# Kernel optimization log

Measured on AMD Instinct MI355X. Metric: run time of the kernel, lower is better.

## Reference

```python
import jax, jax.numpy as jnp
import numpy as np

N = 50000      # num nodes (spots)
E = 800000     # num edges before self-loops
IN = 3000      # input_dim (HVGs)
HID = 512      # hidden_dim
LAT = 30       # latent_dim
HEADS = 1
NEG_SLOPE = 0.2


def setup_inputs() -> dict:
    key = jax.random.key(0)
    ks = jax.random.split(key, 8)
    x = jax.random.normal(ks[0], (N, IN), jnp.float32)
    edge_index = jax.random.randint(ks[1], (2, E), 0, N)
    edge_attr = jax.random.uniform(ks[2], (E,), jnp.float32)
    # parameters (Xavier-ish scales)
    enc_w1 = jax.random.normal(ks[3], (HID, IN), jnp.float32) * (1.0 / np.sqrt(IN))
    enc_b1 = jnp.zeros((HID,), jnp.float32)
    gat_w = jax.random.normal(ks[4], (HID, HEADS * LAT), jnp.float32) * (1.0 / np.sqrt(HID))
    gat_att = jax.random.normal(ks[5], (HEADS, 2 * LAT), jnp.float32) * 0.1
    gat_b = jnp.zeros((LAT,), jnp.float32)
    dec_w1 = jax.random.normal(ks[6], (HID, LAT), jnp.float32) * (1.0 / np.sqrt(LAT))
    dec_b1 = jnp.zeros((HID,), jnp.float32)
    dec_b2 = jnp.zeros((IN,), jnp.float32)
    return dict(x=x, edge_index=edge_index, edge_attr=edge_attr,
                enc_w1=enc_w1, enc_b1=enc_b1, gat_w=gat_w, gat_att=gat_att,
                gat_b=gat_b, dec_w1=dec_w1, dec_b1=dec_b1, dec_b2=dec_b2)


def _gat_layer(h, src, dst, eattr, gat_w, gat_att, gat_b):
    """GAT layer: Eq.5-7, concat=False (mean over heads), multiplicative edge_attr."""
    xh = (h @ gat_w).reshape(N, HEADS, LAT)          # W h, per head
    x_i = xh[dst]                                     # target node feats (E+N, H, LAT)
    x_j = xh[src]                                     # source node feats
    att_i, att_j = gat_att[:, :LAT], gat_att[:, LAT:]
    # e_ij = LeakyReLU(a^T [Wh_i || Wh_j])
    alpha = jnp.einsum('ehc,hc->eh', x_i, att_i) + jnp.einsum('ehc,hc->eh', x_j, att_j)
    alpha = jax.nn.leaky_relu(alpha, NEG_SLOPE)
    alpha = alpha * eattr[:, None]                    # edge weight applied pre-softmax
    # segment softmax over incoming edges of each target node (self-loops ensure non-empty)
    amax = jax.ops.segment_max(alpha, dst, num_segments=N)
    alpha = jnp.exp(alpha - amax[dst])
    denom = jax.ops.segment_sum(alpha, dst, num_segments=N)
    alpha = alpha / (denom[dst] + 1e-16)
    # h'_i = sum_j alpha_ij * W h_j
    msg = x_j * alpha[:, :, None]                     # (E+N, H, LAT)
    out = jax.ops.segment_sum(msg, dst, num_segments=N)  # (N, H, LAT)
    return out.mean(axis=1) + gat_b                   # concat=False -> mean over heads


def reference(x, edge_index, edge_attr, enc_w1, enc_b1, gat_w, gat_att, gat_b,
              dec_w1, dec_b1, dec_b2):
    # add self-loops with fill_value=1.0
    loops = jnp.arange(N, dtype=edge_index.dtype)
    src = jnp.concatenate([edge_index[0], loops])
    dst = jnp.concatenate([edge_index[1], loops])
    eattr = jnp.concatenate([edge_attr, jnp.ones((N,), edge_attr.dtype)])

    # encoder: fc1 -> ELU -> GAT -> ELU
    h = jax.nn.elu(x @ enc_w1.T + enc_b1)
    z = jax.nn.elu(_gat_layer(h, src, dst, eattr, gat_w, gat_att, gat_b))

    # decoder: fc1 -> ELU -> tied fc2 (W^b = W^T, own bias)
    hd = jax.nn.elu(z @ dec_w1.T + dec_b1)
    x_recon = hd @ enc_w1 + dec_b2
    return (x_recon, z)
```

## Files before the change

### kernel.cpp

```cpp
#include <hip/hip_runtime.h>
#include <hip/hip_bf16.h>
#include <math.h>

#define N_NODES 50000
#define E_EDGES 800000
#define ET (E_EDGES + N_NODES)
#define IN_DIM 3000
#define HID 512
#define LAT 30
#define XH_STRIDE 32
#define NEG_SLOPE 0.2f
#define KPAD 3072
#define ENC_NT 94
#define DEC_NT 16
#define APITCH 40

typedef __bf16 bfv8 __attribute__((ext_vector_type(8)));
typedef float f32x4 __attribute__((ext_vector_type(4)));

__device__ __forceinline__ float eluf(float x) { return x > 0.f ? x : expm1f(x); }

__device__ __forceinline__ unsigned fkey(float f) {
    unsigned u = __float_as_uint(f);
    return (u & 0x80000000u) ? ~u : (u | 0x80000000u);
}
__device__ __forceinline__ float funkey(unsigned k) {
    unsigned u = (k & 0x80000000u) ? (k ^ 0x80000000u) : ~k;
    return __uint_as_float(u);
}

__global__ void k_init(float* __restrict__ zbuf, unsigned* __restrict__ amax, float* __restrict__ denom) {
    int gid = blockIdx.x * 256 + threadIdx.x;
    if (gid < N_NODES * XH_STRIDE) zbuf[gid] = 0.f;
    if (gid < N_NODES) { amax[gid] = 0u; denom[gid] = 0.f; }
}

__global__ void k_transpose_w(const float* __restrict__ w, float* __restrict__ wt) {
    int idx = blockIdx.x * 256 + threadIdx.x;
    if (idx < HID * LAT) {
        int j = idx / LAT, c = idx % LAT;
        wt[c * HID + j] = w[idx];
    }
}

__global__ void k_conv_w(const float* __restrict__ w, __bf16* __restrict__ w1b, __bf16* __restrict__ w1bt) {
    int idx = blockIdx.x * 256 + threadIdx.x;
    if (idx >= HID * KPAD) return;
    int j = idx / KPAD, k = idx - j * KPAD;
    float v = (k < IN_DIM) ? w[(size_t)j * IN_DIM + k] : 0.f;
    __bf16 b = (__bf16)v;
    w1b[(size_t)j * KPAD + k] = b;
    w1bt[(size_t)k * HID + j] = b;
}

__global__ __launch_bounds__(256)
void k_enc_gemm(const float* __restrict__ A, const __bf16* __restrict__ Bb,
                const float* __restrict__ bias, float* __restrict__ C) {
    __shared__ __bf16 As[2][128 * APITCH];
    __shared__ __bf16 Bs[3][4096];
    const int tid = threadIdx.x;
    const int lane = tid & 63, wv = tid >> 6;
    const int wr = wv >> 1, wc = wv & 1;
    const int l16 = lane & 15, lh = lane >> 4;
    const int p = ((int)blockIdx.y >> 2) * 8 + (int)blockIdx.x;
    if (p > 390) return;
    const int i0 = p * 128;
    const int c0 = ((int)blockIdx.y & 3) * 128;

    const int arow = tid >> 2, akc = tid & 3;
    const int r0 = i0 + arow, r1 = i0 + arow + 64;
    const float* apA = A + (size_t)(r0 < N_NODES ? r0 : N_NODES - 1) * IN_DIM + akc * 8;
    const float* apB = A + (size_t)(r1 < N_NODES ? r1 : N_NODES - 1) * IN_DIM + akc * 8;

    f32x4 acc[4][4] = {};
    float4 a00, a01, a10, a11;

    auto stageB = [&](int kt, int b) {
#pragma unroll
        for (int s = 0; s < 2; ++s) {
            int g = wv * 2 + s;
            int ks = g >> 1;
            int col = (g & 1) * 64 + (lane ^ (ks << 1));
            const __bf16* src = Bb + (size_t)(c0 + col) * KPAD + kt + ks * 8;
            __builtin_amdgcn_global_load_lds(
                (const __attribute__((address_space(1))) void*)src,
                (__attribute__((address_space(3))) void*)(&Bs[b][(size_t)g * 512]),
                16, 0, 0);
        }
    };
    auto loadA = [&](int kt) {
        a00 = a01 = a10 = a11 = make_float4(0.f, 0.f, 0.f, 0.f);
        if (kt + akc * 8 < IN_DIM) {
            const float4* p0 = (const float4*)(apA + kt);
            a00 = p0[0]; a01 = p0[1];
            const float4* p1 = (const float4*)(apB + kt);
            a10 = p1[0]; a11 = p1[1];
        }
    };
    auto writeA = [&](int b) {
        bfv8 pk;
        pk[0] = (__bf16)a00.x; pk[1] = (__bf16)a00.y; pk[2] = (__bf16)a00.z; pk[3] = (__bf16)a00.w;
        pk[4] = (__bf16)a01.x; pk[5] = (__bf16)a01.y; pk[6] = (__bf16)a01.z; pk[7] = (__bf16)a01.w;
        *(bfv8*)&As[b][(size_t)arow * APITCH + akc * 8] = pk;
        pk[0] = (__bf16)a10.x; pk[1] = (__bf16)a10.y; pk[2] = (__bf16)a10.z; pk[3] = (__bf16)a10.w;
        pk[4] = (__bf16)a11.x; pk[5] = (__bf16)a11.y; pk[6] = (__bf16)a11.z; pk[7] = (__bf16)a11.w;
        *(bfv8*)&As[b][(size_t)(arow + 64) * APITCH + akc * 8] = pk;
    };

    stageB(0, 0);
    stageB(32, 1);
    loadA(0);
    writeA(0);
    asm volatile("s_waitcnt vmcnt(0) lgkmcnt(0)" ::: "memory");
    __builtin_amdgcn_s_barrier();
    __builtin_amdgcn_sched_barrier(0);

    int acur = 0;
    for (int t = 0; t < ENC_NT; ++t) {
        const int bt = t % 3;
        const bool nxt1 = (t + 1) < ENC_NT, nxt2 = (t + 2) < ENC_NT;
        if (nxt1) loadA((t + 1) * 32);
        if (nxt2) stageB((t + 2) * 32, (t + 2) % 3);

        bfv8 af[4], bfr[4];
#pragma unroll
        for (int mi = 0; mi < 4; ++mi)
            af[mi] = *(const bfv8*)&As[acur][(size_t)(wr * 64 + mi * 16 + l16) * APITCH + lh * 8];
#pragma unroll
        for (int ni = 0; ni < 4; ++ni)
            bfr[ni] = *(const bfv8*)&Bs[bt][((size_t)lh * 128 + wc * 64 + ((ni * 16 + l16) ^ (lh << 1))) * 8];
#pragma unroll
        for (int mi = 0; mi < 4; ++mi)
#pragma unroll
            for (int ni = 0; ni < 4; ++ni)
                acc[mi][ni] = __builtin_amdgcn_mfma_f32_16x16x32_bf16(af[mi], bfr[ni], acc[mi][ni], 0, 0, 0);
        if (nxt1) writeA(acur ^ 1);
        if (nxt2) {
            asm volatile("s_waitcnt vmcnt(2) lgkmcnt(0)" ::: "memory");
        } else {
            asm volatile("s_waitcnt vmcnt(0) lgkmcnt(0)" ::: "memory");
        }
        __builtin_amdgcn_s_barrier();
        __builtin_amdgcn_sched_barrier(0);
        acur ^= 1;
    }

#pragma unroll
    for (int ni = 0; ni < 4; ++ni) {
        int col = c0 + wc * 64 + ni * 16 + l16;
        float bv = bias[col];
#pragma unroll
        for (int mi = 0; mi < 4; ++mi) {
            int row0 = i0 + wr * 64 + mi * 16 + lh * 4;
#pragma unroll
            for (int r = 0; r < 4; ++r) {
                int row = row0 + r;
                if (row < N_NODES)
                    C[(size_t)row * HID + col] = eluf(acc[mi][ni][r] + bv);
            }
        }
    }
}

__global__ __launch_bounds__(256)
void k_dec_gemm(const __bf16* __restrict__ Ab, const __bf16* __restrict__ Bt,
                const float* __restrict__ bias, float* __restrict__ C) {
    __shared__ __bf16 As[3][4096];
    __shared__ __bf16 Bs[3][4096];
    const int tid = threadIdx.x;
    const int lane = tid & 63, wv = tid >> 6;
    const int wr = wv >> 1, wc = wv & 1;
    const int l16 = lane & 15, lh = lane >> 4;
    const int p = ((int)blockIdx.y / 24) * 8 + (int)blockIdx.x;
    if (p > 390) return;
    const int i0 = p * 128;
    const int c0 = ((int)blockIdx.y % 24) * 128;

    f32x4 acc[4][4] = {};

    auto stage = [&](int kt, int b) {
#pragma unroll
        for (int s = 0; s < 2; ++s) {
            int g = wv * 2 + s;
            int ks = g >> 1;
            int rc = (g & 1) * 64 + (lane ^ (ks << 1));
            int row = i0 + rc; if (row >= N_NODES) row = N_NODES - 1;
            const __bf16* srcA = Ab + (size_t)row * HID + kt + ks * 8;
            __builtin_amdgcn_global_load_lds(
                (const __attribute__((address_space(1))) void*)srcA,
                (__attribute__((address_space(3))) void*)(&As[b][(size_t)g * 512]),
                16, 0, 0);
            const __bf16* srcB = Bt + (size_t)(c0 + rc) * HID + kt + ks * 8;
            __builtin_amdgcn_global_load_lds(
                (const __attribute__((address_space(1))) void*)srcB,
                (__attribute__((address_space(3))) void*)(&Bs[b][(size_t)g * 512]),
                16, 0, 0);
        }
    };

    stage(0, 0);
    stage(32, 1);
    asm volatile("s_waitcnt vmcnt(4) lgkmcnt(0)" ::: "memory");
    __builtin_amdgcn_s_barrier();
    __builtin_amdgcn_sched_barrier(0);

#pragma unroll 1
    for (int t = 0; t < DEC_NT; ++t) {
        const int bt = t % 3;
        if (t + 2 < DEC_NT) stage((t + 2) * 32, (t + 2) % 3);
        bfv8 af[4], bfr[4];
#pragma unroll
        for (int mi = 0; mi < 4; ++mi)
            af[mi] = *(const bfv8*)&As[bt][((size_t)lh * 128 + wr * 64 + ((mi * 16 + l16) ^ (lh << 1))) * 8];
#pragma unroll
        for (int ni = 0; ni < 4; ++ni)
            bfr[ni] = *(const bfv8*)&Bs[bt][((size_t)lh * 128 + wc * 64 + ((ni * 16 + l16) ^ (lh << 1))) * 8];
#pragma unroll
        for (int mi = 0; mi < 4; ++mi)
#pragma unroll
            for (int ni = 0; ni < 4; ++ni)
                acc[mi][ni] = __builtin_amdgcn_mfma_f32_16x16x32_bf16(af[mi], bfr[ni], acc[mi][ni], 0, 0, 0);
        if (t + 2 < DEC_NT) {
            asm volatile("s_waitcnt vmcnt(4) lgkmcnt(0)" ::: "memory");
        } else {
            asm volatile("s_waitcnt vmcnt(0) lgkmcnt(0)" ::: "memory");
        }
        __builtin_amdgcn_s_barrier();
        __builtin_amdgcn_sched_barrier(0);
    }

#pragma unroll
    for (int ni = 0; ni < 4; ++ni) {
        int col = c0 + wc * 64 + ni * 16 + l16;
        if (col >= IN_DIM) continue;
        float bv = bias[col];
#pragma unroll
        for (int mi = 0; mi < 4; ++mi) {
            int row0 = i0 + wr * 64 + mi * 16 + lh * 4;
#pragma unroll
            for (int r = 0; r < 4; ++r) {
                int row = row0 + r;
                if (row < N_NODES)
                    C[(size_t)row * IN_DIM + col] = acc[mi][ni][r] + bv;
            }
        }
    }
}

__global__ __launch_bounds__(256)
void k_gat_proj(const float* __restrict__ h, const float* __restrict__ gat_w,
                const float* __restrict__ gat_att,
                float* __restrict__ xh, float* __restrict__ si, float* __restrict__ sj) {
    __shared__ float gwl[HID * LAT];
    __shared__ float atl[2 * LAT];
    int tid = threadIdx.x;
    for (int i = tid; i < HID * LAT; i += 256) gwl[i] = gat_w[i];
    if (tid < 2 * LAT) atl[tid] = gat_att[tid];
    __syncthreads();
    int c = tid & 31;
    bool act = c < LAT;
    for (int it = 0; it < 16; ++it) {
        int n = blockIdx.x * 128 + it * 8 + (tid >> 5);
        if (n >= N_NODES) continue;
        float accv = 0.f;
        const float4* h4 = (const float4*)(h + (size_t)n * HID);
#pragma unroll 4
        for (int j4 = 0; j4 < HID / 4; ++j4) {
            float4 hv = h4[j4];
            if (act) {
                int b = j4 * 4 * LAT + c;
                accv = fmaf(hv.x, gwl[b], accv);
                accv = fmaf(hv.y, gwl[b + LAT], accv);
                accv = fmaf(hv.z, gwl[b + 2 * LAT], accv);
                accv = fmaf(hv.w, gwl[b + 3 * LAT], accv);
            }
        }
        float xhv = act ? accv : 0.f;
        xh[(size_t)n * XH_STRIDE + c] = xhv;
        float sip = act ? atl[c] * xhv : 0.f;
        float sjp = act ? atl[LAT + c] * xhv : 0.f;
#pragma unroll
        for (int off = 16; off > 0; off >>= 1) {
            sip += __shfl_down(sip, off, 32);
            sjp += __shfl_down(sjp, off, 32);
        }
        if (c == 0) { si[n] = sip; sj[n] = sjp; }
    }
}

__global__ void k_edge_alpha(const int* __restrict__ ei, const float* __restrict__ eattr,
                             const float* __restrict__ si, const float* __restrict__ sj,
                             float* __restrict__ alphaE, unsigned* __restrict__ amax) {
    int e = blockIdx.x * 256 + threadIdx.x;
    if (e >= ET) return;
    int s, d; float w;
    if (e < E_EDGES) { s = ei[e]; d = ei[E_EDGES + e]; w = eattr[e]; }
    else { s = d = e - E_EDGES; w = 1.f; }
    float a = si[d] + sj[s];
    a = a >= 0.f ? a : NEG_SLOPE * a;
    a *= w;
    alphaE[e] = a;
    atomicMax(&amax[d], fkey(a));
}

__global__ void k_edge_exp(const int* __restrict__ ei, float* __restrict__ alphaE,
                           const unsigned* __restrict__ amax, float* __restrict__ denom) {
    int e = blockIdx.x * 256 + threadIdx.x;
    if (e >= ET) return;
    int d = (e < E_EDGES) ? ei[E_EDGES + e] : (e - E_EDGES);
    float v = expf(alphaE[e] - funkey(amax[d]));
    alphaE[e] = v;
    atomicAdd(&denom[d], v);
}

__global__ void k_edge_scatter(const int* __restrict__ ei, const float* __restrict__ alphaE,
                               const float* __restrict__ xh, float* __restrict__ zbuf) {
    int gid = blockIdx.x * 256 + threadIdx.x;
    int e = gid >> 5, c = gid & 31;
    if (e >= ET || c >= LAT) return;
    int s, d;
    if (e < E_EDGES) { s = ei[e]; d = ei[E_EDGES + e]; }
    else { s = d = e - E_EDGES; }
    atomicAdd(&zbuf[(size_t)d * XH_STRIDE + c], alphaE[e] * xh[(size_t)s * XH_STRIDE + c]);
}

__global__ void k_z(const float* __restrict__ gat_b, const float* __restrict__ denom,
                    float* __restrict__ zbuf, float* __restrict__ zout) {
    int gid = blockIdx.x * 256 + threadIdx.x;
    int n = gid >> 5, c = gid & 31;
    if (n >= N_NODES) return;
    if (c < LAT) {
        float v = eluf(zbuf[gid] / (denom[n] + 1e-16f) + gat_b[c]);
        zbuf[gid] = v;
        zout[(size_t)n * LAT + c] = v;
    }
}

__global__ __launch_bounds__(256)
void k_dec1(const float* __restrict__ zbuf, const float* __restrict__ wt,
            const float* __restrict__ b, __bf16* __restrict__ hdb) {
    int gid = blockIdx.x * 256 + threadIdx.x;
    if (gid >= N_NODES * HID) return;
    int j = gid & (HID - 1);
    size_t i = (size_t)(gid >> 9);
    float acc = b[j];
#pragma unroll
    for (int c = 0; c < LAT; ++c)
        acc = fmaf(zbuf[i * XH_STRIDE + c], wt[c * HID + j], acc);
    hdb[gid] = (__bf16)eluf(acc);
}

extern "C" void kernel_launch(void* const* d_in, const int* in_sizes, int n_in,
                              void* d_out, int out_size, void* d_ws, size_t ws_size,
                              hipStream_t stream) {
    const float* x      = (const float*)d_in[0];
    const int*   ei     = (const int*)d_in[1];
    const float* eattr  = (const float*)d_in[2];
    const float* enc_w1 = (const float*)d_in[3];
    const float* enc_b1 = (const float*)d_in[4];
    const float* gat_w  = (const float*)d_in[5];
    const float* gat_att= (const float*)d_in[6];
    const float* gat_b  = (const float*)d_in[7];
    const float* dec_w1 = (const float*)d_in[8];
    const float* dec_b1 = (const float*)d_in[9];
    const float* dec_b2 = (const float*)d_in[10];

    float* out  = (float*)d_out;
    float* xrec = out;
    float* zout = out + (size_t)N_NODES * IN_DIM;

    float* ws = (float*)d_ws;
    float*    h      = ws;
    float*    xh     = ws + 25600000;
    float*    zbuf   = ws + 27200000;
    float*    si     = ws + 28800000;
    float*    sj     = ws + 28850000;
    unsigned* amax   = (unsigned*)(ws + 28900000);
    float*    denom  = ws + 28950000;
    float*    alphaE = ws + 29000000;
    float*    wt     = ws + 29850000;
    __bf16*   w1b    = (__bf16*)(ws + 29865360);
    __bf16*   w1bt   = (__bf16*)(ws + 30651792);
    __bf16*   hdb    = (__bf16*)h;

    (void)in_sizes; (void)n_in; (void)out_size; (void)ws_size;

    k_init<<<(N_NODES * XH_STRIDE + 255) / 256, 256, 0, stream>>>(zbuf, amax, denom);
    k_transpose_w<<<(HID * LAT + 255) / 256, 256, 0, stream>>>(dec_w1, wt);
    k_conv_w<<<(HID * KPAD + 255) / 256, 256, 0, stream>>>(enc_w1, w1b, w1bt);

    {
        dim3 g(8, 196);
        k_enc_gemm<<<g, 256, 0, stream>>>(x, w1b, enc_b1, h);
    }

    k_gat_proj<<<(N_NODES + 127) / 128, 256, 0, stream>>>(h, gat_w, gat_att, xh, si, sj);
    k_edge_alpha<<<(ET + 255) / 256, 256, 0, stream>>>(ei, eattr, si, sj, alphaE, amax);
    k_edge_exp<<<(ET + 255) / 256, 256, 0, stream>>>(ei, alphaE, amax, denom);
    k_edge_scatter<<<((size_t)ET * 32 + 255) / 256, 256, 0, stream>>>(ei, alphaE, xh, zbuf);
    k_z<<<(N_NODES * 32 + 255) / 256, 256, 0, stream>>>(gat_b, denom, zbuf, zout);
    k_dec1<<<(N_NODES * HID + 255) / 256, 256, 0, stream>>>(zbuf, wt, dec_b1, hdb);

    {
        dim3 g(8, 1176);
        k_dec_gemm<<<g, 256, 0, stream>>>(hdb, w1bt, dec_b2, xrec);
    }
}
```

Measured before the change: 1.825 ms.

## Build CSR by destination for fused GAT softmax aggregation and restructure encoder A staging

Result: faster. 1.771 ms (-3.0%).

```diff
diff --git a/kernel.cpp b/kernel.cpp
--- a/kernel.cpp
+++ b/kernel.cpp
@@ -13,26 +13,16 @@
 #define KPAD 3072
 #define ENC_NT 94
 #define DEC_NT 16
-#define APITCH 40
+#define APLANE 1040
 
 typedef __bf16 bfv8 __attribute__((ext_vector_type(8)));
 typedef float f32x4 __attribute__((ext_vector_type(4)));
 
 __device__ __forceinline__ float eluf(float x) { return x > 0.f ? x : expm1f(x); }
 
-__device__ __forceinline__ unsigned fkey(float f) {
-    unsigned u = __float_as_uint(f);
-    return (u & 0x80000000u) ? ~u : (u | 0x80000000u);
-}
-__device__ __forceinline__ float funkey(unsigned k) {
-    unsigned u = (k & 0x80000000u) ? (k ^ 0x80000000u) : ~k;
-    return __uint_as_float(u);
-}
-
-__global__ void k_init(float* __restrict__ zbuf, unsigned* __restrict__ amax, float* __restrict__ denom) {
+__global__ void k_init(unsigned* __restrict__ hist) {
     int gid = blockIdx.x * 256 + threadIdx.x;
-    if (gid < N_NODES * XH_STRIDE) zbuf[gid] = 0.f;
-    if (gid < N_NODES) { amax[gid] = 0u; denom[gid] = 0.f; }
+    if (gid < N_NODES) hist[gid] = 0u;
 }
 
 __global__ void k_transpose_w(const float* __restrict__ w, float* __restrict__ wt) {
@@ -56,7 +46,7 @@
 __global__ __launch_bounds__(256)
 void k_enc_gemm(const float* __restrict__ A, const __bf16* __restrict__ Bb,
                 const float* __restrict__ bias, float* __restrict__ C) {
-    __shared__ __bf16 As[2][128 * APITCH];
+    __shared__ __bf16 As[2][4 * APLANE];
     __shared__ __bf16 Bs[3][4096];
     const int tid = threadIdx.x;
     const int lane = tid & 63, wv = tid >> 6;
@@ -73,14 +63,14 @@
     const float* apB = A + (size_t)(r1 < N_NODES ? r1 : N_NODES - 1) * IN_DIM + akc * 8;
 
     f32x4 acc[4][4] = {};
-    float4 a00, a01, a10, a11;
+    float4 R0[4], R1[4];
 
     auto stageB = [&](int kt, int b) {
 #pragma unroll
         for (int s = 0; s < 2; ++s) {
             int g = wv * 2 + s;
+            int col = (g & 1) * 64 + lane;
             int ks = g >> 1;
-            int col = (g & 1) * 64 + (lane ^ (ks << 1));
             const __bf16* src = Bb + (size_t)(c0 + col) * KPAD + kt + ks * 8;
             __builtin_amdgcn_global_load_lds(
                 (const __attribute__((address_space(1))) void*)src,
@@ -88,61 +78,86 @@
                 16, 0, 0);
         }
     };
-    auto loadA = [&](int kt) {
-        a00 = a01 = a10 = a11 = make_float4(0.f, 0.f, 0.f, 0.f);
+    auto loadA = [&](int kt, float4* R) {
+        R[0] = R[1] = R[2] = R[3] = make_float4(0.f, 0.f, 0.f, 0.f);
         if (kt + akc * 8 < IN_DIM) {
             const float4* p0 = (const float4*)(apA + kt);
-            a00 = p0[0]; a01 = p0[1];
+            R[0] = p0[0]; R[1] = p0[1];
             const float4* p1 = (const float4*)(apB + kt);
-            a10 = p1[0]; a11 = p1[1];
+            R[2] = p1[0]; R[3] = p1[1];
         }
     };
-    auto writeA = [&](int b) {
+    auto writeA = [&](const float4* R, int b) {
         bfv8 pk;
-        pk[0] = (__bf16)a00.x; pk[1] = (__bf16)a00.y; pk[2] = (__bf16)a00.z; pk[3] = (__bf16)a00.w;
-        pk[4] = (__bf16)a01.x; pk[5] = (__bf16)a01.y; pk[6] = (__bf16)a01.z; pk[7] = (__bf16)a01.w;
-        *(bfv8*)&As[b][(size_t)arow * APITCH + akc * 8] = pk;
-        pk[0] = (__bf16)a10.x; pk[1] = (__bf16)a10.y; pk[2] = (__bf16)a10.z; pk[3] = (__bf16)a10.w;
-        pk[4] = (__bf16)a11.x; pk[5] = (__bf16)a11.y; pk[6] = (__bf16)a11.z; pk[7] = (__bf16)a11.w;
-        *(bfv8*)&As[b][(size_t)(arow + 64) * APITCH + akc * 8] = pk;
+        pk[0] = (__bf16)R[0].x; pk[1] = (__bf16)R[0].y; pk[2] = (__bf16)R[0].z; pk[3] = (__bf16)R[0].w;
+        pk[4] = (__bf16)R[1].x; pk[5] = (__bf16)R[1].y; pk[6] = (__bf16)R[1].z; pk[7] = (__bf16)R[1].w;
+        *(bfv8*)&As[b][(size_t)akc * APLANE + arow * 8] = pk;
+        pk[0] = (__bf16)R[2].x; pk[1] = (__bf16)R[2].y; pk[2] = (__bf16)R[2].z; pk[3] = (__bf16)R[2].w;
+        pk[4] = (__bf16)R[3].x; pk[5] = (__bf16)R[3].y; pk[6] = (__bf16)R[3].z; pk[7] = (__bf16)R[3].w;
+        *(bfv8*)&As[b][(size_t)akc * APLANE + (arow + 64) * 8] = pk;
     };
-
+    auto mfmaStep = [&](int tb, int bb) {
+        bfv8 af[4], bfr[4];
+#pragma unroll
+        for (int mi = 0; mi < 4; ++mi)
+            af[mi] = *(const bfv8*)&As[tb][(size_t)lh * APLANE + (wr * 64 + mi * 16 + l16) * 8];
+#pragma unroll
+        for (int ni = 0; ni < 4; ++ni)
+            bfr[ni] = *(const bfv8*)&Bs[bb][((size_t)lh * 128 + wc * 64 + ni * 16 + l16) * 8];
+#pragma unroll
+        for (int mi = 0; mi < 4; ++mi)
+#pragma unroll
+            for (int ni = 0; ni < 4; ++ni)
+                acc[mi][ni] = __builtin_amdgcn_mfma_f32_16x16x32_bf16(af[mi], bfr[ni], acc[mi][ni], 0, 0, 0);
+    };
+
+    loadA(0, R0);
     stageB(0, 0);
     stageB(32, 1);
-    loadA(0);
-    writeA(0);
-    asm volatile("s_waitcnt vmcnt(0) lgkmcnt(0)" ::: "memory");
+    loadA(32, R1);
+    asm volatile("s_waitcnt vmcnt(8)" ::: "memory");
+    __builtin_amdgcn_sched_barrier(0);
+    writeA(R0, 0);
+    asm volatile("s_waitcnt vmcnt(6) lgkmcnt(0)" ::: "memory");
     __builtin_amdgcn_s_barrier();
     __builtin_amdgcn_sched_barrier(0);
 
-    int acur = 0;
-    for (int t = 0; t < ENC_NT; ++t) {
-        const int bt = t % 3;
-        const bool nxt1 = (t + 1) < ENC_NT, nxt2 = (t + 2) < ENC_NT;
-        if (nxt1) loadA((t + 1) * 32);
-        if (nxt2) stageB((t + 2) * 32, (t + 2) % 3);
-
-        bfv8 af[4], bfr[4];
-#pragma unroll
-        for (int mi = 0; mi < 4; ++mi)
-            af[mi] = *(const bfv8*)&As[acur][(size_t)(wr * 64 + mi * 16 + l16) * APITCH + lh * 8];
-#pragma unroll
-        for (int ni = 0; ni < 4; ++ni)
-            bfr[ni] = *(const bfv8*)&Bs[bt][((size_t)lh * 128 + wc * 64 + ((ni * 16 + l16) ^ (lh << 1))) * 8];
-#pragma unroll
-        for (int mi = 0; mi < 4; ++mi)
-#pragma unroll
-            for (int ni = 0; ni < 4; ++ni)
-                acc[mi][ni] = __builtin_amdgcn_mfma_f32_16x16x32_bf16(af[mi], bfr[ni], acc[mi][ni], 0, 0, 0);
-        if (nxt1) writeA(acur ^ 1);
-        if (nxt2) {
-            asm volatile("s_waitcnt vmcnt(2) lgkmcnt(0)" ::: "memory");
-        } else {
-            asm volatile("s_waitcnt vmcnt(0) lgkmcnt(0)" ::: "memory");
-        }
-        __builtin_amdgcn_s_barrier();
-        __builtin_amdgcn_sched_barrier(0);
-        acur ^= 1;
+    for (int tt = 0; tt < ENC_NT; tt += 2) {
+        {
+            const int t = tt;
+            const bool ld = (t + 2) < ENC_NT;
+            if (ld) {
+                loadA((t + 2) * 32, R0);
+                stageB((t + 2) * 32, (t + 2) % 3);
+            }
+            mfmaStep(t & 1, t % 3);
+            if (ld) asm volatile("s_waitcnt vmcnt(6)" ::: "memory");
+            else    asm volatile("s_waitcnt vmcnt(0)" ::: "memory");
+            __builtin_amdgcn_sched_barrier(0);
+            writeA(R1, (t + 1) & 1);
+            asm volatile("s_waitcnt lgkmcnt(0)" ::: "memory");
+            __builtin_amdgcn_s_barrier();
+            __builtin_amdgcn_sched_barrier(0);
+        }
+        {
+            const int t = tt + 1;
+            const bool ld = (t + 2) < ENC_NT;
+            const bool wr1 = (t + 1) < ENC_NT;
+            if (ld) {
+                loadA((t + 2) * 32, R1);
+                stageB((t + 2) * 32, (t + 2) % 3);
+            }
+            mfmaStep(t & 1, t % 3);
+            if (wr1) {
+                if (ld) asm volatile("s_waitcnt vmcnt(6)" ::: "memory");
+                else    asm volatile("s_waitcnt vmcnt(0)" ::: "memory");
+                __builtin_amdgcn_sched_barrier(0);
+                writeA(R0, (t + 1) & 1);
+                asm volatile("s_waitcnt lgkmcnt(0)" ::: "memory");
+                __builtin_amdgcn_s_barrier();
+                __builtin_amdgcn_sched_barrier(0);
+            }
+        }
     }
 
 #pragma unroll
@@ -183,7 +198,7 @@
         for (int s = 0; s < 2; ++s) {
             int g = wv * 2 + s;
             int ks = g >> 1;
-            int rc = (g & 1) * 64 + (lane ^ (ks << 1));
+            int rc = (g & 1) * 64 + lane;
             int row = i0 + rc; if (row >= N_NODES) row = N_NODES - 1;
             const __bf16* srcA = Ab + (size_t)row * HID + kt + ks * 8;
             __builtin_amdgcn_global_load_lds(
@@ -211,10 +226,10 @@
         bfv8 af[4], bfr[4];
 #pragma unroll
         for (int mi = 0; mi < 4; ++mi)
-            af[mi] = *(const bfv8*)&As[bt][((size_t)lh * 128 + wr * 64 + ((mi * 16 + l16) ^ (lh << 1))) * 8];
+            af[mi] = *(const bfv8*)&As[bt][((size_t)lh * 128 + wr * 64 + mi * 16 + l16) * 8];
 #pragma unroll
         for (int ni = 0; ni < 4; ++ni)
-            bfr[ni] = *(const bfv8*)&Bs[bt][((size_t)lh * 128 + wc * 64 + ((ni * 16 + l16) ^ (lh << 1))) * 8];
+            bfr[ni] = *(const bfv8*)&Bs[bt][((size_t)lh * 128 + wc * 64 + ni * 16 + l16) * 8];
 #pragma unroll
         for (int mi = 0; mi < 4; ++mi)
 #pragma unroll
@@ -288,50 +303,102 @@
     }
 }
 
-__global__ void k_edge_alpha(const int* __restrict__ ei, const float* __restrict__ eattr,
-                             const float* __restrict__ si, const float* __restrict__ sj,
-                             float* __restrict__ alphaE, unsigned* __restrict__ amax) {
+__global__ void k_hist(const int* __restrict__ ei, unsigned* __restrict__ hist) {
+    int e = blockIdx.x * 256 + threadIdx.x;
+    if (e >= ET) return;
+    int d = (e < E_EDGES) ? ei[E_EDGES + e] : (e - E_EDGES);
+    atomicAdd(&hist[d], 1u);
+}
+
+__global__ __launch_bounds__(1024)
+void k_scan(const unsigned* __restrict__ hist, unsigned* __restrict__ off, unsigned* __restrict__ cursor) {
+    __shared__ unsigned part[1024];
+    const int tid = threadIdx.x;
+    const int b = tid * 49;
+    const int e = (b + 49 < N_NODES) ? b + 49 : N_NODES;
+    unsigned s = 0;
+    for (int i = b; i < e; ++i) s += hist[i];
+    part[tid] = s;
+    __syncthreads();
+    for (int d = 1; d < 1024; d <<= 1) {
+        unsigned v = (tid >= d) ? part[tid - d] : 0u;
+        __syncthreads();
+        part[tid] += v;
+        __syncthreads();
+    }
+    unsigned run = (tid > 0) ? part[tid - 1] : 0u;
+    for (int i = b; i < e; ++i) {
+        off[i] = run; cursor[i] = run;
+        run += hist[i];
+    }
+    if (tid == 1023) off[N_NODES] = run;
+}
+
+__global__ void k_fill(const int* __restrict__ ei, const float* __restrict__ eattr,
+                       unsigned* __restrict__ cursor, int* __restrict__ csr_src,
+                       float* __restrict__ csr_w) {
     int e = blockIdx.x * 256 + threadIdx.x;
     if (e >= ET) return;
     int s, d; float w;
     if (e < E_EDGES) { s = ei[e]; d = ei[E_EDGES + e]; w = eattr[e]; }
     else { s = d = e - E_EDGES; w = 1.f; }
-    float a = si[d] + sj[s];
-    a = a >= 0.f ? a : NEG_SLOPE * a;
-    a *= w;
-    alphaE[e] = a;
-    atomicMax(&amax[d], fkey(a));
-}
-
-__global__ void k_edge_exp(const int* __restrict__ ei, float* __restrict__ alphaE,
-                           const unsigned* __restrict__ amax, float* __restrict__ denom) {
-    int e = blockIdx.x * 256 + threadIdx.x;
-    if (e >= ET) return;
-    int d = (e < E_EDGES) ? ei[E_EDGES + e] : (e - E_EDGES);
-    float v = expf(alphaE[e] - funkey(amax[d]));
-    alphaE[e] = v;
-    atomicAdd(&denom[d], v);
-}
-
-__global__ void k_edge_scatter(const int* __restrict__ ei, const float* __restrict__ alphaE,
-                               const float* __restrict__ xh, float* __restrict__ zbuf) {
-    int gid = blockIdx.x * 256 + threadIdx.x;
-    int e = gid >> 5, c = gid & 31;
-    if (e >= ET || c >= LAT) return;
-    int s, d;
-    if (e < E_EDGES) { s = ei[e]; d = ei[E_EDGES + e]; }
-    else { s = d = e - E_EDGES; }
-    atomicAdd(&zbuf[(size_t)d * XH_STRIDE + c], alphaE[e] * xh[(size_t)s * XH_STRIDE + c]);
-}
-
-__global__ void k_z(const float* __restrict__ gat_b, const float* __restrict__ denom,
-                    float* __restrict__ zbuf, float* __restrict__ zout) {
-    int gid = blockIdx.x * 256 + threadIdx.x;
-    int n = gid >> 5, c = gid & 31;
+    unsigned pos = atomicAdd(&cursor[d], 1u);
+    csr_src[pos] = s;
+    csr_w[pos] = w;
+}
+
+__global__ __launch_bounds__(256)
+void k_gat_agg(const unsigned* __restrict__ off, const int* __restrict__ csr_src,
+               const float* __restrict__ csr_w, const float* __restrict__ si,
+               const float* __restrict__ sj, const float* __restrict__ xh,
+               const float* __restrict__ gat_b,
+               float* __restrict__ zbuf, float* __restrict__ zout) {
+    const int n = blockIdx.x * 4 + (threadIdx.x >> 6);
     if (n >= N_NODES) return;
-    if (c < LAT) {
-        float v = eluf(zbuf[gid] / (denom[n] + 1e-16f) + gat_b[c]);
-        zbuf[gid] = v;
+    const int lane = threadIdx.x & 63;
+    const int beg = (int)off[n], end = (int)off[n + 1];
+    const float s_i = si[n];
+    const int c = lane & 31;
+    const int half = lane >> 5;
+
+    float m = -1e30f;
+    for (int j = beg + lane; j < end; j += 64) {
+        int s = csr_src[j];
+        float a = s_i + sj[s];
+        a = a >= 0.f ? a : NEG_SLOPE * a;
+        a *= csr_w[j];
+        m = fmaxf(m, a);
+    }
+#pragma unroll
+    for (int o = 32; o > 0; o >>= 1) m = fmaxf(m, __shfl_xor(m, o));
+
+    float denom = 0.f, acc = 0.f;
+    for (int base = beg; base < end; base += 64) {
+        int j = base + lane;
+        float v = 0.f; int s = 0;
+        if (j < end) {
+            s = csr_src[j];
+            float a = s_i + sj[s];
+            a = a >= 0.f ? a : NEG_SLOPE * a;
+            a *= csr_w[j];
+            v = __expf(a - m);
+        }
+        denom += v;
+        int cnt = end - base; if (cnt > 64) cnt = 64;
+        for (int q = 0; q < cnt; q += 2) {
+            int src_lane = q + half;
+            float vq = __shfl(v, src_lane);
+            int sq = __shfl(s, src_lane);
+            acc = fmaf(vq, xh[(size_t)sq * XH_STRIDE + c], acc);
+        }
+    }
+#pragma unroll
+    for (int o = 32; o > 0; o >>= 1) denom += __shfl_xor(denom, o);
+    acc += __shfl_xor(acc, 32);
+
+    if (lane < LAT) {
+        float v = eluf(acc / (denom + 1e-16f) + gat_b[c]);
+        zbuf[(size_t)n * XH_STRIDE + c] = v;
         zout[(size_t)n * LAT + c] = v;
     }
 }
@@ -370,35 +437,37 @@
     float* zout = out + (size_t)N_NODES * IN_DIM;
 
     float* ws = (float*)d_ws;
-    float*    h      = ws;
-    float*    xh     = ws + 25600000;
-    float*    zbuf   = ws + 27200000;
-    float*    si     = ws + 28800000;
-    float*    sj     = ws + 28850000;
-    unsigned* amax   = (unsigned*)(ws + 28900000);
-    float*    denom  = ws + 28950000;
-    float*    alphaE = ws + 29000000;
-    float*    wt     = ws + 29850000;
-    __bf16*   w1b    = (__bf16*)(ws + 29865360);
-    __bf16*   w1bt   = (__bf16*)(ws + 30651792);
-    __bf16*   hdb    = (__bf16*)h;
+    float*    h       = ws;
+    float*    xh      = ws + 25600000;
+    float*    zbuf    = ws + 27200000;
+    float*    si      = ws + 28800000;
+    float*    sj      = ws + 28850000;
+    float*    wt      = ws + 28900000;
+    __bf16*   w1b     = (__bf16*)(ws + 28915360);
+    __bf16*   w1bt    = (__bf16*)(ws + 29701792);
+    unsigned* hist    = (unsigned*)(ws + 30488224);
+    unsigned* csr_off = (unsigned*)(ws + 30538224);
+    unsigned* cursor  = (unsigned*)(ws + 30588226);
+    int*      csr_src = (int*)(ws + 30638226);
+    float*    csr_w   = (float*)(ws + 31488226);
+    __bf16*   hdb     = (__bf16*)h;
 
     (void)in_sizes; (void)n_in; (void)out_size; (void)ws_size;
 
-    k_init<<<(N_NODES * XH_STRIDE + 255) / 256, 256, 0, stream>>>(zbuf, amax, denom);
+    k_init<<<(N_NODES + 255) / 256, 256, 0, stream>>>(hist);
     k_transpose_w<<<(HID * LAT + 255) / 256, 256, 0, stream>>>(dec_w1, wt);
     k_conv_w<<<(HID * KPAD + 255) / 256, 256, 0, stream>>>(enc_w1, w1b, w1bt);
+    k_hist<<<(ET + 255) / 256, 256, 0, stream>>>(ei, hist);
 
     {
         dim3 g(8, 196);
         k_enc_gemm<<<g, 256, 0, stream>>>(x, w1b, enc_b1, h);
     }
 
+    k_scan<<<1, 1024, 0, stream>>>(hist, csr_off, cursor);
+    k_fill<<<(ET + 255) / 256, 256, 0, stream>>>(ei, eattr, cursor, csr_src, csr_w);
     k_gat_proj<<<(N_NODES + 127) / 128, 256, 0, stream>>>(h, gat_w, gat_att, xh, si, sj);
-    k_edge_alpha<<<(ET + 255) / 256, 256, 0, stream>>>(ei, eattr, si, sj, alphaE, amax);
-    k_edge_exp<<<(ET + 255) / 256, 256, 0, stream>>>(ei, alphaE, amax, denom);
-    k_edge_scatter<<<((size_t)ET * 32 + 255) / 256, 256, 0, stream>>>(ei, alphaE, xh, zbuf);
-    k_z<<<(N_NODES * 32 + 255) / 256, 256, 0, stream>>>(gat_b, denom, zbuf, zout);
+    k_gat_agg<<<(N_NODES + 3) / 4, 256, 0, stream>>>(csr_off, csr_src, csr_w, si, sj, xh, gat_b, zbuf, zout);
     k_dec1<<<(N_NODES * HID + 255) / 256, 256, 0, stream>>>(zbuf, wt, dec_b1, hdb);
 
     {
```
